# Performance work log

Measured on AMD Instinct MI355X. Metric: run time of the kernel, lower is better.

## Reference

```python
import jax, jax.numpy as jnp
import numpy as np


def adder2d(x, w, stride=1, padding=0):
    """AdderNet conv: out = -sum_{ci,kh,kw} |x_patch - w|, supports groups.
    x: [B,Cin,H,W], w: [Cout, Cin//G, K, K]. Loops only over K*K kernel taps."""
    B, Cin, H, W = x.shape
    Cout, Cin_g, K, _ = w.shape
    G = Cin // Cin_g
    Co_g = Cout // G
    xp = jnp.pad(x, ((0, 0), (0, 0), (padding, padding), (padding, padding)))
    Ho = (H + 2 * padding - K) // stride + 1
    Wo = (W + 2 * padding - K) // stride + 1
    wg = w.reshape(G, Co_g, Cin_g, K, K)
    out = jnp.zeros((B, Cout, Ho, Wo), x.dtype)
    for kh in range(K):
        for kw in range(K):
            xs = jax.lax.slice(
                xp, (0, 0, kh, kw),
                (B, Cin, kh + stride * (Ho - 1) + 1, kw + stride * (Wo - 1) + 1),
                (1, 1, stride, stride))  # [B,Cin,Ho,Wo]
            xs = xs.reshape(B, G, 1, Cin_g, Ho, Wo)
            wt = wg[:, :, :, kh, kw][None, :, :, :, None, None]  # [1,G,Co_g,Cin_g,1,1]
            out = out - jnp.abs(xs - wt).sum(3).reshape(B, Cout, Ho, Wo)
    return out


def bn(x, g, b, m, v, eps=1e-5):
    inv = g / jnp.sqrt(v + eps)
    return x * inv[None, :, None, None] + (b - m * inv)[None, :, None, None]


def setup_inputs() -> dict:
    key = jax.random.key(0)
    ks = jax.random.split(key, 18)
    d = {}
    d["x"] = jax.random.normal(ks[0], (8, 256, 28, 28), jnp.float32)
    d["w1"] = jax.random.normal(ks[1], (64, 256, 1, 1), jnp.float32) * 0.05
    d["w_peg"] = jax.random.normal(ks[2], (64, 1, 3, 3), jnp.float32) * 0.05
    d["w2"] = jax.random.normal(ks[3], (64, 64, 3, 3), jnp.float32) * 0.05
    d["w3"] = jax.random.normal(ks[4], (256, 64, 1, 1), jnp.float32) * 0.05
    for i, (c, tag) in enumerate([(64, "1"), (64, "2"), (256, "3")]):
        d["g" + tag] = jax.random.uniform(ks[5 + 4 * i], (c,), jnp.float32, 0.5, 1.5)
        d["b" + tag] = jax.random.normal(ks[6 + 4 * i], (c,), jnp.float32) * 0.1
        d["m" + tag] = jax.random.normal(ks[7 + 4 * i], (c,), jnp.float32) * 0.1
        d["v" + tag] = jax.random.uniform(ks[8 + 4 * i], (c,), jnp.float32, 0.5, 1.5)
    return d


def reference(x, w1, w_peg, w2, w3, g1, b1, m1, v1, g2, b2, m2, v2, g3, b3, m3, v3):
    residual = x  # downsample is Identity (stride=1, inplanes==outplanes)
    h = adder2d(x, w1)                       # 1x1 adder conv 256->64
    h = adder2d(h, w_peg, stride=1, padding=1)  # PEG: depthwise 3x3 adder conv
    h = jax.nn.relu(bn(h, g1, b1, m1, v1))
    h = adder2d(h, w2, padding=1)            # 3x3 adder conv 64->64
    h = jax.nn.relu(bn(h, g2, b2, m2, v2))
    h = adder2d(h, w3)                       # 1x1 adder conv 64->256
    h = bn(h, g3, b3, m3, v3)
    return jax.nn.relu(h + residual)
```

## Files before the change

kernel.cpp:

```cpp
#include <hip/hip_runtime.h>
#include <math.h>

#define PR 30
#define PC 32

__device__ __forceinline__ void tap3(const float4 a, const float2 b,
                                     const float w0, const float w1, const float w2,
                                     float4& acc) {
    acc.x += fabsf(a.x - w0) + fabsf(a.y - w1) + fabsf(a.z - w2);
    acc.y += fabsf(a.y - w0) + fabsf(a.z - w1) + fabsf(a.w - w2);
    acc.z += fabsf(a.z - w0) + fabsf(a.w - w1) + fabsf(b.x - w2);
    acc.w += fabsf(a.w - w0) + fabsf(b.x - w1) + fabsf(b.y - w2);
}

__global__ __launch_bounds__(448) void ka_fused(const float* __restrict__ x,
                                                const float* __restrict__ w1,
                                                const float* __restrict__ wpeg,
                                                const float* __restrict__ w2,
                                                const float* __restrict__ w3,
                                                const float* __restrict__ g1,
                                                const float* __restrict__ b1,
                                                const float* __restrict__ m1,
                                                const float* __restrict__ v1,
                                                float* __restrict__ h2p,
                                                float* __restrict__ w2t,
                                                float* __restrict__ w3t) {
    __shared__ __align__(16) float smem[3072];
    float* wsA = smem;
    float* h1t = smem + 1024;
    const int tid    = threadIdx.x;
    const int cobase = blockIdx.x * 4;
    const int yh     = blockIdx.y;
    const int n      = blockIdx.z;
    const int co     = tid / 112;
    const int rem    = tid % 112;
    const int row    = rem / 7;
    const int q      = rem % 7;

    {
        const int bid3 = blockIdx.x + 16 * (blockIdx.y + 2 * blockIdx.z);
        const int tg = bid3 * 448 + tid;
        if (tg < 36864) {
            int r = tg >> 6, c2 = tg & 63;
            w2t[tg] = w2[(size_t)c2 * 576 + r];
        } else if (tg < 53248) {
            int i = tg - 36864;
            int ci = i >> 8, c2 = i & 255;
            w3t[i] = w3[(size_t)c2 * 64 + ci];
        }
    }

    for (int idx = tid; idx < 1024; idx += 448) {
        int c2 = idx >> 8, ci = idx & 255;
        wsA[ci * 4 + c2] = w1[(size_t)(cobase + c2) * 256 + ci];
    }
    for (int idx = tid; idx < 512; idx += 448)
        ((float4*)h1t)[idx] = make_float4(0.f, 0.f, 0.f, 0.f);
    __syncthreads();

    const int gy = yh * 14 - 1 + row;
    if (gy >= 0 && gy < 28) {
        float4 acc = {0.f, 0.f, 0.f, 0.f};
        const float* xp = x + (size_t)n * 256 * 784 + gy * 28 + q * 4;
        #pragma unroll 8
        for (int ci = 0; ci < 256; ++ci) {
            float4 u = *(const float4*)(xp + (size_t)ci * 784);
            float w  = wsA[ci * 4 + co];
            acc.x += fabsf(u.x - w); acc.y += fabsf(u.y - w);
            acc.z += fabsf(u.z - w); acc.w += fabsf(u.w - w);
        }
        float* hd = h1t + co * 512 + row * 32 + 1 + q * 4;
        hd[0] = -acc.x; hd[1] = -acc.y; hd[2] = -acc.z; hd[3] = -acc.w;
    }
    __syncthreads();

    if (row < 14) {
        const int c  = cobase + co;
        const int oy = yh * 14 + row;
        const float* wc = wpeg + c * 9;
        const float* hb = h1t + co * 512 + row * 32 + q * 4;
        float4 acc = {0.f, 0.f, 0.f, 0.f};
        #pragma unroll
        for (int kh = 0; kh < 3; ++kh) {
            float4 a  = *(const float4*)(hb + kh * 32);
            float2 bv = *(const float2*)(hb + kh * 32 + 4);
            tap3(a, bv, wc[kh * 3 + 0], wc[kh * 3 + 1], wc[kh * 3 + 2], acc);
        }
        float inv = g1[c] * rsqrtf(v1[c] + 1e-5f);
        float bb  = b1[c] - m1[c] * inv;
        float* op = h2p + ((size_t)(n * 64 + c) * PR + oy + 1) * PC + 1 + q * 4;
        op[0] = fmaxf(-acc.x * inv + bb, 0.f);
        op[1] = fmaxf(-acc.y * inv + bb, 0.f);
        op[2] = fmaxf(-acc.z * inv + bb, 0.f);
        op[3] = fmaxf(-acc.w * inv + bb, 0.f);
    }
    for (int idx = tid; idx < 352; idx += 448) {
        if (idx < 224) {
            int rr = idx >> 4, k = idx & 15;
            int cc = k >> 2, kk = k & 3;
            int col = kk ? 28 + kk : 0;
            h2p[((size_t)(n * 64 + cobase + cc) * PR + yh * 14 + 1 + rr) * PC + col] = 0.f;
        } else {
            int j = idx - 224;
            int cc = j >> 5, col = j & 31;
            int prow = yh ? 29 : 0;
            h2p[((size_t)(n * 64 + cobase + cc) * PR + prow) * PC + col] = 0.f;
        }
    }
}

__global__ __launch_bounds__(512) void k3_part(const float* __restrict__ h2p,
                                               const float* __restrict__ w2t,
                                               float* __restrict__ h3part) {
    __shared__ __align__(16) float h2t[3456];
    __shared__ __align__(16) float wt[9792];
    const int tid  = threadIdx.x;
    const int lane = tid & 63;
    const int oct  = __builtin_amdgcn_readfirstlane(tid >> 6);
    const int col  = lane & 31;
    const int cih  = lane >> 5;
    const int Y0   = blockIdx.x * 4;
    const int ciQ  = blockIdx.y;
    const int n    = blockIdx.z;

    for (int i = tid; i < 768; i += 512) {
        int ci = i / 48, rem = i % 48;
        int r = rem >> 3, c4 = rem & 7;
        *(float4*)(h2t + ci * 216 + r * 36 + c4 * 4) =
            *(const float4*)(h2p + ((size_t)(n * 64 + ciQ * 16 + ci) * PR + Y0 + r) * PC + c4 * 4);
    }
    for (int i = tid; i < 2304; i += 512) {
        int row = i >> 4, c4 = i & 15;
        *(float4*)(wt + row * 68 + c4 * 4) =
            *(const float4*)(w2t + ((size_t)ciQ * 144 + row) * 64 + c4 * 4);
    }
    __syncthreads();

    float acc[4][8];
    #pragma unroll
    for (int r = 0; r < 4; ++r)
        #pragma unroll
        for (int j = 0; j < 8; ++j) acc[r][j] = 0.f;

    #pragma unroll 2
    for (int i = 0; i < 8; ++i) {
        const int ci = cih * 8 + i;
        float win[6][3];
        #pragma unroll
        for (int r = 0; r < 6; ++r)
            #pragma unroll
            for (int kw = 0; kw < 3; ++kw)
                win[r][kw] = h2t[ci * 216 + r * 36 + col + kw];
        const float* wrow = wt + ci * 612 + oct * 8;
        #pragma unroll
        for (int kh = 0; kh < 3; ++kh) {
            #pragma unroll
            for (int kw = 0; kw < 3; ++kw) {
                float4 wa = *(const float4*)(wrow + (kh * 3 + kw) * 68);
                float4 wb = *(const float4*)(wrow + (kh * 3 + kw) * 68 + 4);
                #pragma unroll
                for (int r = 0; r < 4; ++r) {
                    const float xv = win[r + kh][kw];
                    acc[r][0] += fabsf(xv - wa.x); acc[r][1] += fabsf(xv - wa.y);
                    acc[r][2] += fabsf(xv - wa.z); acc[r][3] += fabsf(xv - wa.w);
                    acc[r][4] += fabsf(xv - wb.x); acc[r][5] += fabsf(xv - wb.y);
                    acc[r][6] += fabsf(xv - wb.z); acc[r][7] += fabsf(xv - wb.w);
                }
            }
        }
    }
    #pragma unroll
    for (int r = 0; r < 4; ++r)
        #pragma unroll
        for (int j = 0; j < 8; ++j)
            acc[r][j] += __shfl_xor(acc[r][j], 32, 64);

    if (cih == 0 && col < 28) {
        #pragma unroll
        for (int r = 0; r < 4; ++r)
            #pragma unroll
            for (int j = 0; j < 8; ++j)
                h3part[(((size_t)ciQ * 8 + n) * 64 + oct * 8 + j) * 784 + (Y0 + r) * 28 + col] = acc[r][j];
    }
}

__global__ __launch_bounds__(512) void k6_fused(const float* __restrict__ h3part,
                                                const float* __restrict__ w3t,
                                                const float* __restrict__ x,
                                                const float* __restrict__ g2,
                                                const float* __restrict__ b2,
                                                const float* __restrict__ m2,
                                                const float* __restrict__ v2,
                                                const float* __restrict__ g3,
                                                const float* __restrict__ b3,
                                                const float* __restrict__ m3,
                                                const float* __restrict__ v3,
                                                float* __restrict__ out) {
    __shared__ __align__(16) float h3t[2048];
    __shared__ __align__(16) float w3s[16896];
    const int tid = threadIdx.x;
    const int Y   = blockIdx.x;
    const int n   = blockIdx.y;

    if (tid < 448) {
        const int co = tid / 7, c4 = tid % 7;
        size_t base = ((size_t)n * 64 + co) * 784 + Y * 28 + c4 * 4;
        const size_t qstride = (size_t)8 * 64 * 784;
        float4 s = *(const float4*)(h3part + base);
        #pragma unroll
        for (int qq = 1; qq < 4; ++qq) {
            float4 t = *(const float4*)(h3part + qq * qstride + base);
            s.x += t.x; s.y += t.y; s.z += t.z; s.w += t.w;
        }
        float inv = g2[co] * rsqrtf(v2[co] + 1e-5f);
        float bb  = b2[co] - m2[co] * inv;
        float4 o;
        o.x = fmaxf(-s.x * inv + bb, 0.f);
        o.y = fmaxf(-s.y * inv + bb, 0.f);
        o.z = fmaxf(-s.z * inv + bb, 0.f);
        o.w = fmaxf(-s.w * inv + bb, 0.f);
        *(float4*)(h3t + co * 32 + c4 * 4) = o;
    }
    for (int iq = tid; iq < 4096; iq += 512) {
        int ci = iq >> 6, cq = iq & 63;
        *(float4*)(w3s + ci * 264 + cq * 4) =
            *(const float4*)(w3t + (size_t)ci * 256 + cq * 4);
    }
    __syncthreads();

    {
        const int bl = tid & 63;
        const int pg = tid >> 6;
        float4 c0 = {0,0,0,0}, c1 = c0, c2 = c0, c3 = c0;
        const float* hb = h3t + pg * 4;
        const float* wb = w3s + bl * 4;
        #pragma unroll 8
        for (int ci = 0; ci < 64; ++ci) {
            float4 h = *(const float4*)(hb + ci * 32);
            float4 w = *(const float4*)(wb + ci * 264);
            c0.x += fabsf(h.x - w.x); c0.y += fabsf(h.y - w.x); c0.z += fabsf(h.z - w.x); c0.w += fabsf(h.w - w.x);
            c1.x += fabsf(h.x - w.y); c1.y += fabsf(h.y - w.y); c1.z += fabsf(h.z - w.y); c1.w += fabsf(h.w - w.y);
            c2.x += fabsf(h.x - w.z); c2.y += fabsf(h.y - w.z); c2.z += fabsf(h.z - w.z); c2.w += fabsf(h.w - w.z);
            c3.x += fabsf(h.x - w.w); c3.y += fabsf(h.y - w.w); c3.z += fabsf(h.z - w.w); c3.w += fabsf(h.w - w.w);
        }
        if (pg < 7) {
            float4 accs[4] = {c0, c1, c2, c3};
            #pragma unroll
            for (int j = 0; j < 4; ++j) {
                const int co = bl * 4 + j;
                float inv = g3[co] * rsqrtf(v3[co] + 1e-5f);
                float bb  = b3[co] - m3[co] * inv;
                size_t obase = ((size_t)n * 256 + co) * 784 + Y * 28 + pg * 4;
                float4 r = *(const float4*)(x + obase);
                float4 o;
                o.x = fmaxf(-accs[j].x * inv + bb + r.x, 0.f);
                o.y = fmaxf(-accs[j].y * inv + bb + r.y, 0.f);
                o.z = fmaxf(-accs[j].z * inv + bb + r.z, 0.f);
                o.w = fmaxf(-accs[j].w * inv + bb + r.w, 0.f);
                *(float4*)(out + obase) = o;
            }
        }
    }
}

extern "C" void kernel_launch(void* const* d_in, const int* in_sizes, int n_in,
                              void* d_out, int out_size, void* d_ws, size_t ws_size,
                              hipStream_t stream) {
    const float* x  = (const float*)d_in[0];
    const float* w1 = (const float*)d_in[1];
    const float* wp = (const float*)d_in[2];
    const float* w2 = (const float*)d_in[3];
    const float* w3 = (const float*)d_in[4];
    const float* g1 = (const float*)d_in[5];
    const float* b1 = (const float*)d_in[6];
    const float* m1 = (const float*)d_in[7];
    const float* v1 = (const float*)d_in[8];
    const float* g2 = (const float*)d_in[9];
    const float* b2 = (const float*)d_in[10];
    const float* m2 = (const float*)d_in[11];
    const float* v2 = (const float*)d_in[12];
    const float* g3 = (const float*)d_in[13];
    const float* b3 = (const float*)d_in[14];
    const float* m3 = (const float*)d_in[15];
    const float* v3 = (const float*)d_in[16];
    float* out = (float*)d_out;

    float* wsf     = (float*)d_ws;
    float* h2p     = wsf;
    float* w2t     = wsf + 491520;
    float* w3t     = wsf + 528384;
    float* h3part  = wsf + 544768;

    ka_fused<<<dim3(16, 2, 8), 448, 0, stream>>>(x, w1, wp, w2, w3,
                                                 g1, b1, m1, v1, h2p, w2t, w3t);
    k3_part<<<dim3(7, 4, 8), 512, 0, stream>>>(h2p, w2t, h3part);
    k6_fused<<<dim3(28, 8), 512, 0, stream>>>(h3part, w3t, x,
                                              g2, b2, m2, v2, g3, b3, m3, v3, out);
}
```

Measured before the change: 63.46 us.

## Split 3x3 adder conv into 8 channel groups with wave-uniform global weights

The 3x3 adder conv kernel now splits input channels into 8 groups of 8 instead of 4 groups of 16, doubling the grid. Each half-wave handles two output rows instead of splitting channels, which removes the cross-lane shuffle reduction. The weights are re-laid out in the prep kernel so each wave reads its 8 output channels contiguously straight from global memory, so the shared-memory weight tile is dropped. The cost is twice as many partial sums written to and re-summed by the final kernel, and weight reads that now rely on scalar or cached global loads.

Measured after the change: 65.87 us. 1.04x slower.

```diff
diff --git a/kernel.cpp b/kernel.cpp
--- a/kernel.cpp
+++ b/kernel.cpp
@@ -23,7 +23,7 @@
                                                 const float* __restrict__ m1,
                                                 const float* __restrict__ v1,
                                                 float* __restrict__ h2p,
-                                                float* __restrict__ w2t,
+                                                float* __restrict__ w2q,
                                                 float* __restrict__ w3t) {
     __shared__ __align__(16) float smem[3072];
     float* wsA = smem;
@@ -41,8 +41,12 @@
         const int bid3 = blockIdx.x + 16 * (blockIdx.y + 2 * blockIdx.z);
         const int tg = bid3 * 448 + tid;
         if (tg < 36864) {
-            int r = tg >> 6, c2 = tg & 63;
-            w2t[tg] = w2[(size_t)c2 * 576 + r];
+            int co_l = tg & 7;
+            int tap  = (tg >> 3) % 9;
+            int ci_l = (tg / 72) & 7;
+            int oct  = (tg / 576) & 7;
+            int ciQ  = tg / 4608;
+            w2q[tg] = w2[(size_t)(oct * 8 + co_l) * 576 + (ciQ * 8 + ci_l) * 9 + tap];
         } else if (tg < 53248) {
             int i = tg - 36864;
             int ci = i >> 8, c2 = i & 255;
@@ -110,77 +114,66 @@
 }
 
 __global__ __launch_bounds__(512) void k3_part(const float* __restrict__ h2p,
-                                               const float* __restrict__ w2t,
+                                               const float* __restrict__ w2q,
                                                float* __restrict__ h3part) {
-    __shared__ __align__(16) float h2t[3456];
-    __shared__ __align__(16) float wt[9792];
+    __shared__ __align__(16) float h2t[8][224];
     const int tid  = threadIdx.x;
     const int lane = tid & 63;
     const int oct  = __builtin_amdgcn_readfirstlane(tid >> 6);
     const int col  = lane & 31;
-    const int cih  = lane >> 5;
+    const int rh   = lane >> 5;
     const int Y0   = blockIdx.x * 4;
     const int ciQ  = blockIdx.y;
     const int n    = blockIdx.z;
 
-    for (int i = tid; i < 768; i += 512) {
+    for (int i = tid; i < 384; i += 512) {
         int ci = i / 48, rem = i % 48;
         int r = rem >> 3, c4 = rem & 7;
-        *(float4*)(h2t + ci * 216 + r * 36 + c4 * 4) =
-            *(const float4*)(h2p + ((size_t)(n * 64 + ciQ * 16 + ci) * PR + Y0 + r) * PC + c4 * 4);
-    }
-    for (int i = tid; i < 2304; i += 512) {
-        int row = i >> 4, c4 = i & 15;
-        *(float4*)(wt + row * 68 + c4 * 4) =
-            *(const float4*)(w2t + ((size_t)ciQ * 144 + row) * 64 + c4 * 4);
-    }
-    __syncthreads();
-
-    float acc[4][8];
+        *(float4*)(&h2t[ci][r * 36 + c4 * 4]) =
+            *(const float4*)(h2p + ((size_t)(n * 64 + ciQ * 8 + ci) * PR + Y0 + r) * PC + c4 * 4);
+    }
+    __syncthreads();
+
+    const float* wq = w2q + (size_t)(ciQ * 8 + oct) * 576;
+
+    float acc[2][8];
     #pragma unroll
-    for (int r = 0; r < 4; ++r)
+    for (int r = 0; r < 2; ++r)
         #pragma unroll
         for (int j = 0; j < 8; ++j) acc[r][j] = 0.f;
 
-    #pragma unroll 2
-    for (int i = 0; i < 8; ++i) {
-        const int ci = cih * 8 + i;
-        float win[6][3];
-        #pragma unroll
-        for (int r = 0; r < 6; ++r)
+    for (int ci = 0; ci < 8; ++ci) {
+        float win[4][3];
+        #pragma unroll
+        for (int r = 0; r < 4; ++r)
             #pragma unroll
             for (int kw = 0; kw < 3; ++kw)
-                win[r][kw] = h2t[ci * 216 + r * 36 + col + kw];
-        const float* wrow = wt + ci * 612 + oct * 8;
+                win[r][kw] = h2t[ci][(rh * 2 + r) * 36 + col + kw];
+        const float* w = wq + ci * 72;
         #pragma unroll
         for (int kh = 0; kh < 3; ++kh) {
             #pragma unroll
             for (int kw = 0; kw < 3; ++kw) {
-                float4 wa = *(const float4*)(wrow + (kh * 3 + kw) * 68);
-                float4 wb = *(const float4*)(wrow + (kh * 3 + kw) * 68 + 4);
+                const float* wt = w + (kh * 3 + kw) * 8;
                 #pragma unroll
-                for (int r = 0; r < 4; ++r) {
-                    const float xv = win[r + kh][kw];
-                    acc[r][0] += fabsf(xv - wa.x); acc[r][1] += fabsf(xv - wa.y);
-                    acc[r][2] += fabsf(xv - wa.z); acc[r][3] += fabsf(xv - wa.w);
-                    acc[r][4] += fabsf(xv - wb.x); acc[r][5] += fabsf(xv - wb.y);
-                    acc[r][6] += fabsf(xv - wb.z); acc[r][7] += fabsf(xv - wb.w);
+                for (int r2 = 0; r2 < 2; ++r2) {
+                    const float xv = win[r2 + kh][kw];
+                    acc[r2][0] += fabsf(xv - wt[0]); acc[r2][1] += fabsf(xv - wt[1]);
+                    acc[r2][2] += fabsf(xv - wt[2]); acc[r2][3] += fabsf(xv - wt[3]);
+                    acc[r2][4] += fabsf(xv - wt[4]); acc[r2][5] += fabsf(xv - wt[5]);
+                    acc[r2][6] += fabsf(xv - wt[6]); acc[r2][7] += fabsf(xv - wt[7]);
                 }
             }
         }
     }
-    #pragma unroll
-    for (int r = 0; r < 4; ++r)
-        #pragma unroll
-        for (int j = 0; j < 8; ++j)
-            acc[r][j] += __shfl_xor(acc[r][j], 32, 64);
-
-    if (cih == 0 && col < 28) {
-        #pragma unroll
-        for (int r = 0; r < 4; ++r)
+
+    if (col < 28) {
+        #pragma unroll
+        for (int r2 = 0; r2 < 2; ++r2)
             #pragma unroll
             for (int j = 0; j < 8; ++j)
-                h3part[(((size_t)ciQ * 8 + n) * 64 + oct * 8 + j) * 784 + (Y0 + r) * 28 + col] = acc[r][j];
+                h3part[(((size_t)ciQ * 8 + n) * 64 + oct * 8 + j) * 784 +
+                       (Y0 + rh * 2 + r2) * 28 + col] = acc[r2][j];
     }
 }
 
@@ -208,7 +201,7 @@
         const size_t qstride = (size_t)8 * 64 * 784;
         float4 s = *(const float4*)(h3part + base);
         #pragma unroll
-        for (int qq = 1; qq < 4; ++qq) {
+        for (int qq = 1; qq < 8; ++qq) {
             float4 t = *(const float4*)(h3part + qq * qstride + base);
             s.x += t.x; s.y += t.y; s.z += t.z; s.w += t.w;
         }
@@ -287,13 +280,13 @@
 
     float* wsf     = (float*)d_ws;
     float* h2p     = wsf;
-    float* w2t     = wsf + 491520;
+    float* w2q     = wsf + 491520;
     float* w3t     = wsf + 528384;
     float* h3part  = wsf + 544768;
 
     ka_fused<<<dim3(16, 2, 8), 448, 0, stream>>>(x, w1, wp, w2, w3,
-                                                 g1, b1, m1, v1, h2p, w2t, w3t);
-    k3_part<<<dim3(7, 4, 8), 512, 0, stream>>>(h2p, w2t, h3part);
+                                                 g1, b1, m1, v1, h2p, w2q, w3t);
+    k3_part<<<dim3(7, 8, 8), 512, 0, stream>>>(h2p, w2q, h3part);
     k6_fused<<<dim3(28, 8), 512, 0, stream>>>(h3part, w3t, x,
                                               g2, b2, m2, v2, g3, b3, m3, v3, out);
 }
```

## Split fused 1x1+PEG kernel, add ci-split reduction, double conv3x3 split

Applied to the files above, without the earlier changes.

The fused first kernel is split into a 1x1 adder kernel that uses a channel-split partial reduction in shared memory, with 16 output channels per block and 896 blocks, and a separate elementwise PEG+BN+ReLU kernel that also zeroes padding and transposes the weights. The 3x3 adder kernel now splits input channels 8 ways instead of 4, giving twice as many blocks, and the final kernel sums 8 partials. The aim is more parallelism and occupancy, since the old launches used only 256 and 224 blocks. In exchange it adds a kernel launch, a global round trip for h1, and more partial-sum traffic.

Result: faster. 59.14 us, median of 2 (-6.8%).

```diff
diff --git a/kernel.cpp b/kernel.cpp
--- a/kernel.cpp
+++ b/kernel.cpp
@@ -13,107 +13,130 @@
     acc.w += fabsf(a.w - w0) + fabsf(b.x - w1) + fabsf(b.y - w2);
 }
 
-__global__ __launch_bounds__(448) void ka_fused(const float* __restrict__ x,
-                                                const float* __restrict__ w1,
-                                                const float* __restrict__ wpeg,
-                                                const float* __restrict__ w2,
-                                                const float* __restrict__ w3,
-                                                const float* __restrict__ g1,
-                                                const float* __restrict__ b1,
-                                                const float* __restrict__ m1,
-                                                const float* __restrict__ v1,
-                                                float* __restrict__ h2p,
-                                                float* __restrict__ w2t,
-                                                float* __restrict__ w3t) {
-    __shared__ __align__(16) float smem[3072];
-    float* wsA = smem;
-    float* h1t = smem + 1024;
+__global__ __launch_bounds__(448) void k1_adder1x1(const float* __restrict__ x,
+                                                   const float* __restrict__ w1,
+                                                   float* __restrict__ h1p) {
+    __shared__ __align__(16) float smem[7168];
+    float*  ws  = smem;
+    float4* pl4 = (float4*)smem;
     const int tid    = threadIdx.x;
-    const int cobase = blockIdx.x * 4;
-    const int yh     = blockIdx.y;
-    const int n      = blockIdx.z;
-    const int co     = tid / 112;
-    const int rem    = tid % 112;
-    const int row    = rem / 7;
-    const int q      = rem % 7;
-
-    {
-        const int bid3 = blockIdx.x + 16 * (blockIdx.y + 2 * blockIdx.z);
-        const int tg = bid3 * 448 + tid;
-        if (tg < 36864) {
-            int r = tg >> 6, c2 = tg & 63;
-            w2t[tg] = w2[(size_t)c2 * 576 + r];
-        } else if (tg < 53248) {
-            int i = tg - 36864;
-            int ci = i >> 8, c2 = i & 255;
-            w3t[i] = w3[(size_t)c2 * 64 + ci];
-        }
-    }
-
-    for (int idx = tid; idx < 1024; idx += 448) {
-        int c2 = idx >> 8, ci = idx & 255;
-        wsA[ci * 4 + c2] = w1[(size_t)(cobase + c2) * 256 + ci];
-    }
-    for (int idx = tid; idx < 512; idx += 448)
-        ((float4*)h1t)[idx] = make_float4(0.f, 0.f, 0.f, 0.f);
-    __syncthreads();
-
-    const int gy = yh * 14 - 1 + row;
-    if (gy >= 0 && gy < 28) {
-        float4 acc = {0.f, 0.f, 0.f, 0.f};
-        const float* xp = x + (size_t)n * 256 * 784 + gy * 28 + q * 4;
-        #pragma unroll 8
-        for (int ci = 0; ci < 256; ++ci) {
-            float4 u = *(const float4*)(xp + (size_t)ci * 784);
-            float w  = wsA[ci * 4 + co];
-            acc.x += fabsf(u.x - w); acc.y += fabsf(u.y - w);
-            acc.z += fabsf(u.z - w); acc.w += fabsf(u.w - w);
-        }
-        float* hd = h1t + co * 512 + row * 32 + 1 + q * 4;
-        hd[0] = -acc.x; hd[1] = -acc.y; hd[2] = -acc.z; hd[3] = -acc.w;
-    }
-    __syncthreads();
-
-    if (row < 14) {
-        const int c  = cobase + co;
-        const int oy = yh * 14 + row;
-        const float* wc = wpeg + c * 9;
-        const float* hb = h1t + co * 512 + row * 32 + q * 4;
-        float4 acc = {0.f, 0.f, 0.f, 0.f};
+    const int cog    = tid & 3;
+    const int pxg    = (tid >> 2) % 7;
+    const int cic    = tid / 28;
+    const int n      = blockIdx.x / 28;
+    const int y      = blockIdx.x % 28;
+    const int px0    = y * 28 + pxg * 4;
+    const int cobase = blockIdx.y * 16;
+
+    for (int idx = tid; idx < 4096; idx += 448) {
+        int co = idx >> 8, ci = idx & 255;
+        ws[ci * 20 + co] = w1[(size_t)(cobase + co) * 256 + ci];
+    }
+    __syncthreads();
+
+    float4 acc0 = {0,0,0,0}, acc1 = acc0, acc2 = acc0, acc3 = acc0;
+    const float* xp = x + ((size_t)n * 256 + cic * 16) * 784 + px0;
+    const float* wp = ws + (cic * 16) * 20 + cog * 4;
+    #pragma unroll 8
+    for (int i = 0; i < 16; ++i) {
+        float4 u = *(const float4*)(xp + (size_t)i * 784);
+        float4 w = *(const float4*)(wp + i * 20);
+        acc0.x += fabsf(u.x - w.x); acc0.y += fabsf(u.y - w.x); acc0.z += fabsf(u.z - w.x); acc0.w += fabsf(u.w - w.x);
+        acc1.x += fabsf(u.x - w.y); acc1.y += fabsf(u.y - w.y); acc1.z += fabsf(u.z - w.y); acc1.w += fabsf(u.w - w.y);
+        acc2.x += fabsf(u.x - w.z); acc2.y += fabsf(u.y - w.z); acc2.z += fabsf(u.z - w.z); acc2.w += fabsf(u.w - w.z);
+        acc3.x += fabsf(u.x - w.w); acc3.y += fabsf(u.y - w.w); acc3.z += fabsf(u.z - w.w); acc3.w += fabsf(u.w - w.w);
+    }
+    __syncthreads();
+    const int pbase = pxg * 16 + cog * 4;
+    pl4[cic * 112 + pbase + 0] = acc0;
+    pl4[cic * 112 + pbase + 1] = acc1;
+    pl4[cic * 112 + pbase + 2] = acc2;
+    pl4[cic * 112 + pbase + 3] = acc3;
+    __syncthreads();
+
+    if (tid < 112) {
+        const int rpxg = tid >> 4;
+        const int rcog = (tid >> 2) & 3;
+        const int j    = tid & 3;
+        const int rb   = rpxg * 16 + rcog * 4 + j;
+        float4 s = pl4[rb];
+        #pragma unroll
+        for (int c = 1; c < 16; ++c) {
+            float4 t = pl4[c * 112 + rb];
+            s.x += t.x; s.y += t.y; s.z += t.z; s.w += t.w;
+        }
+        const int co = cobase + rcog * 4 + j;
+        float* op = h1p + ((size_t)(n * 64 + co) * PR + y + 1) * PC + rpxg * 4 + 1;
+        op[0] = -s.x; op[1] = -s.y; op[2] = -s.z; op[3] = -s.w;
+        if (rpxg == 0) op[-1] = 0.f;
+        if (rpxg == 6) { op[4] = 0.f; op[5] = 0.f; op[6] = 0.f; }
+    }
+    if (y == 0 || y == 27) {
+        const int prow = (y == 0) ? 0 : 29;
+        for (int idx = tid; idx < 512; idx += 448) {
+            int coi = idx >> 5, col = idx & 31;
+            h1p[((size_t)(n * 64 + cobase + coi) * PR + prow) * PC + col] = 0.f;
+        }
+    }
+}
+
+__global__ __launch_bounds__(256) void k2_peg_bn_relu(const float* __restrict__ h1p,
+                                                      const float* __restrict__ wp,
+                                                      const float* __restrict__ w2,
+                                                      const float* __restrict__ w3,
+                                                      const float* __restrict__ g1,
+                                                      const float* __restrict__ b1,
+                                                      const float* __restrict__ m1,
+                                                      const float* __restrict__ v1,
+                                                      float* __restrict__ h2p,
+                                                      float* __restrict__ w2t,
+                                                      float* __restrict__ w3t) {
+    const int t = blockIdx.x * 256 + threadIdx.x;
+    if (t < 100352) {
+        const int pxq = t % 196;
+        const int c   = (t / 196) & 63;
+        const int n   = t / (196 * 64);
+        const int p0  = pxq * 4;
+        const int y   = p0 / 28, xx = p0 % 28;
+        const float* base = h1p + ((size_t)(n * 64 + c) * PR + y) * PC + xx;
+        const float* wc   = wp + c * 9;
+        float4 acc = {0,0,0,0};
         #pragma unroll
         for (int kh = 0; kh < 3; ++kh) {
-            float4 a  = *(const float4*)(hb + kh * 32);
-            float2 bv = *(const float2*)(hb + kh * 32 + 4);
-            tap3(a, bv, wc[kh * 3 + 0], wc[kh * 3 + 1], wc[kh * 3 + 2], acc);
+            float4 a = *(const float4*)(base + kh * PC);
+            float2 b = *(const float2*)(base + kh * PC + 4);
+            tap3(a, b, wc[kh * 3 + 0], wc[kh * 3 + 1], wc[kh * 3 + 2], acc);
         }
         float inv = g1[c] * rsqrtf(v1[c] + 1e-5f);
         float bb  = b1[c] - m1[c] * inv;
-        float* op = h2p + ((size_t)(n * 64 + c) * PR + oy + 1) * PC + 1 + q * 4;
+        float* op = h2p + ((size_t)(n * 64 + c) * PR + y + 1) * PC + xx + 1;
         op[0] = fmaxf(-acc.x * inv + bb, 0.f);
         op[1] = fmaxf(-acc.y * inv + bb, 0.f);
         op[2] = fmaxf(-acc.z * inv + bb, 0.f);
         op[3] = fmaxf(-acc.w * inv + bb, 0.f);
-    }
-    for (int idx = tid; idx < 352; idx += 448) {
-        if (idx < 224) {
-            int rr = idx >> 4, k = idx & 15;
-            int cc = k >> 2, kk = k & 3;
-            int col = kk ? 28 + kk : 0;
-            h2p[((size_t)(n * 64 + cobase + cc) * PR + yh * 14 + 1 + rr) * PC + col] = 0.f;
-        } else {
-            int j = idx - 224;
-            int cc = j >> 5, col = j & 31;
-            int prow = yh ? 29 : 0;
-            h2p[((size_t)(n * 64 + cobase + cc) * PR + prow) * PC + col] = 0.f;
-        }
+    } else if (t < 190464) {
+        int i = t - 100352;
+        int plane = i / 176, r = i % 176;
+        int row, col;
+        if (r < 64) { row = (r >> 5) * 29; col = r & 31; }
+        else { int j = r - 64; row = 1 + (j >> 2); int k = j & 3; col = k ? 28 + k : 0; }
+        h2p[(size_t)plane * (PR * PC) + row * PC + col] = 0.f;
+    } else if (t < 227328) {
+        int i = t - 190464;
+        int r = i >> 6, c2 = i & 63;
+        w2t[i] = w2[(size_t)c2 * 576 + r];
+    } else if (t < 243712) {
+        int i = t - 227328;
+        int ci = i >> 8, c2 = i & 255;
+        w3t[i] = w3[(size_t)c2 * 64 + ci];
     }
 }
 
 __global__ __launch_bounds__(512) void k3_part(const float* __restrict__ h2p,
                                                const float* __restrict__ w2t,
                                                float* __restrict__ h3part) {
-    __shared__ __align__(16) float h2t[3456];
-    __shared__ __align__(16) float wt[9792];
+    __shared__ __align__(16) float h2t[1728];
+    __shared__ __align__(16) float wt[4896];
     const int tid  = threadIdx.x;
     const int lane = tid & 63;
     const int oct  = __builtin_amdgcn_readfirstlane(tid >> 6);
@@ -123,16 +146,16 @@
     const int ciQ  = blockIdx.y;
     const int n    = blockIdx.z;
 
-    for (int i = tid; i < 768; i += 512) {
+    for (int i = tid; i < 384; i += 512) {
         int ci = i / 48, rem = i % 48;
         int r = rem >> 3, c4 = rem & 7;
         *(float4*)(h2t + ci * 216 + r * 36 + c4 * 4) =
-            *(const float4*)(h2p + ((size_t)(n * 64 + ciQ * 16 + ci) * PR + Y0 + r) * PC + c4 * 4);
-    }
-    for (int i = tid; i < 2304; i += 512) {
+            *(const float4*)(h2p + ((size_t)(n * 64 + ciQ * 8 + ci) * PR + Y0 + r) * PC + c4 * 4);
+    }
+    for (int i = tid; i < 1152; i += 512) {
         int row = i >> 4, c4 = i & 15;
         *(float4*)(wt + row * 68 + c4 * 4) =
-            *(const float4*)(w2t + ((size_t)ciQ * 144 + row) * 64 + c4 * 4);
+            *(const float4*)(w2t + ((size_t)ciQ * 72 + row) * 64 + c4 * 4);
     }
     __syncthreads();
 
@@ -142,16 +165,16 @@
         #pragma unroll
         for (int j = 0; j < 8; ++j) acc[r][j] = 0.f;
 
-    #pragma unroll 2
-    for (int i = 0; i < 8; ++i) {
-        const int ci = cih * 8 + i;
+    #pragma unroll
+    for (int i = 0; i < 4; ++i) {
+        const int ci_l = cih * 4 + i;
         float win[6][3];
         #pragma unroll
         for (int r = 0; r < 6; ++r)
             #pragma unroll
             for (int kw = 0; kw < 3; ++kw)
-                win[r][kw] = h2t[ci * 216 + r * 36 + col + kw];
-        const float* wrow = wt + ci * 612 + oct * 8;
+                win[r][kw] = h2t[ci_l * 216 + r * 36 + col + kw];
+        const float* wrow = wt + ci_l * 612 + oct * 8;
         #pragma unroll
         for (int kh = 0; kh < 3; ++kh) {
             #pragma unroll
@@ -208,7 +231,7 @@
         const size_t qstride = (size_t)8 * 64 * 784;
         float4 s = *(const float4*)(h3part + base);
         #pragma unroll
-        for (int qq = 1; qq < 4; ++qq) {
+        for (int qq = 1; qq < 8; ++qq) {
             float4 t = *(const float4*)(h3part + qq * qstride + base);
             s.x += t.x; s.y += t.y; s.z += t.z; s.w += t.w;
         }
@@ -286,14 +309,16 @@
     float* out = (float*)d_out;
 
     float* wsf     = (float*)d_ws;
-    float* h2p     = wsf;
-    float* w2t     = wsf + 491520;
-    float* w3t     = wsf + 528384;
-    float* h3part  = wsf + 544768;
-
-    ka_fused<<<dim3(16, 2, 8), 448, 0, stream>>>(x, w1, wp, w2, w3,
-                                                 g1, b1, m1, v1, h2p, w2t, w3t);
-    k3_part<<<dim3(7, 4, 8), 512, 0, stream>>>(h2p, w2t, h3part);
+    float* h1p     = wsf;
+    float* h2p     = wsf + 491520;
+    float* w2t     = wsf + 983040;
+    float* w3t     = wsf + 1019904;
+    float* h3part  = wsf + 1036288;
+
+    k1_adder1x1<<<dim3(224, 4), 448, 0, stream>>>(x, w1, h1p);
+    k2_peg_bn_relu<<<dim3(952), 256, 0, stream>>>(h1p, wp, w2, w3,
+                                                  g1, b1, m1, v1, h2p, w2t, w3t);
+    k3_part<<<dim3(7, 8, 8), 512, 0, stream>>>(h2p, w2t, h3part);
     k6_fused<<<dim3(28, 8), 512, 0, stream>>>(h3part, w3t, x,
                                               g2, b2, m2, v2, g3, b3, m3, v3, out);
 }
```
